# Performance work log

Measured on AMD Instinct MI355X. Metric: run time of the kernel, lower is better.

Reference implementation:

```python
import jax, jax.numpy as jnp
import numpy as np

B, T, C = 4, 2048, 768
H, KVH, D = 6, 6, 128
HALF = D // 2


def setup_inputs() -> dict:
    key = jax.random.key(0)
    ks = jax.random.split(key, 5)
    x = jax.random.normal(ks[0], (B, T, C), dtype=jnp.float32)
    # true rotary frequencies
    inv_freq = 1.0 / (10000.0 ** (jnp.arange(HALF, dtype=jnp.float32) / HALF))
    ang = jnp.arange(T, dtype=jnp.float32)[:, None] * inv_freq[None, :]  # [T, HALF]
    cos, sin = jnp.cos(ang), jnp.sin(ang)
    s = 0.02
    wq = jax.random.normal(ks[1], (H * D, C), dtype=jnp.float32) * s
    wk = jax.random.normal(ks[2], (KVH * D, C), dtype=jnp.float32) * s
    wv = jax.random.normal(ks[3], (KVH * D, C), dtype=jnp.float32) * s
    wproj = jax.random.normal(ks[4], (C, C), dtype=jnp.float32) * s
    return {"x": x, "cos": cos, "sin": sin, "wq": wq, "wk": wk, "wv": wv, "wproj": wproj}


def _norm(t, eps=1e-6):
    # torch: (x - mean) / (std + eps), std unbiased (ddof=1)
    mean = jnp.mean(t, axis=-1, keepdims=True)
    var = jnp.sum((t - mean) ** 2, axis=-1, keepdims=True) / (t.shape[-1] - 1)
    return (t - mean) / (jnp.sqrt(var) + eps)


def _rope(t, cos, sin):
    # t: [B, T, heads, D]; cos/sin: [T, HALF]
    x1, x2 = t[..., :HALF], t[..., HALF:]
    c = cos[None, :, None, :]
    s = sin[None, :, None, :]
    return jnp.concatenate([x1 * c + x2 * s, -x1 * s + x2 * c], axis=-1)


def reference(x, cos, sin, wq, wk, wv, wproj):
    q = jnp.einsum('btc,oc->bto', x, wq).reshape(B, T, H, D)
    k = jnp.einsum('btc,oc->bto', x, wk).reshape(B, T, KVH, D)
    v = jnp.einsum('btc,oc->bto', x, wv).reshape(B, T, KVH, D)
    q = _norm(_rope(q, cos, sin))
    k = _norm(_rope(k, cos, sin))
    # -> [B, heads, T, D]
    q = q.transpose(0, 2, 1, 3)
    k = k.transpose(0, 2, 1, 3)
    v = v.transpose(0, 2, 1, 3)
    # nrep = H // KVH == 1, repeat_kv is a no-op here
    scale = 1.0 / jnp.sqrt(jnp.float32(D))
    scores = jnp.einsum('bhtd,bhsd->bhts', q, k) * scale  # [B,H,T,T]
    causal = jnp.tril(jnp.ones((T, T), dtype=bool))
    scores = jnp.where(causal[None, None], scores, jnp.float32(-1e30))
    attn = jax.nn.softmax(scores, axis=-1)
    y = jnp.einsum('bhts,bhsd->bhtd', attn, v)
    y = y.transpose(0, 2, 1, 3).reshape(B, T, H * D)
    return jnp.einsum('bto,co->btc', y, wproj)
```

## Files before the change

### kernel.cpp

```cpp
#include <hip/hip_runtime.h>

#define BB 4
#define TT 2048
#define CC 768
#define HH 6
#define DD 128
#define BT (BB * TT)
#define HALF 64
#define NBH (BB * HH)
#define QKSCALE 0.12753785627919282f

typedef __bf16 v8bf __attribute__((ext_vector_type(8)));
typedef float f32x4 __attribute__((ext_vector_type(4)));

__device__ __forceinline__ unsigned short f2b(float f) {
  union { float f; unsigned u; } v; v.f = f;
  unsigned r = v.u + 0x7FFFu + ((v.u >> 16) & 1u);
  return (unsigned short)(r >> 16);
}
__device__ __forceinline__ float b2f(unsigned short u) {
  union { unsigned u; float f; } v; v.u = (unsigned)u << 16;
  return v.f;
}
__device__ __forceinline__ unsigned pk2(float f0, float f1) {
  union { float f; unsigned u; } a, b; a.f = f1; b.f = f0;
  return __builtin_amdgcn_perm(a.u, b.u, 0x07060302u);
}
__device__ __forceinline__ float ex2(float x) {
  float r; asm("v_exp_f32 %0, %1" : "=v"(r) : "v"(x)); return r;
}

__device__ __forceinline__ void load_lds16(const void* g, void* l) {
  __builtin_amdgcn_global_load_lds(
      (const __attribute__((address_space(1))) unsigned int*)g,
      (__attribute__((address_space(3))) unsigned int*)(unsigned int)(unsigned long long)(l),
      16, 0, 0);
}

__global__ __launch_bounds__(256) void cvt_all_kernel(const float* __restrict__ x,
                                                      const float* __restrict__ w0,
                                                      const float* __restrict__ w1,
                                                      const float* __restrict__ w2,
                                                      const float* __restrict__ w3,
                                                      unsigned short* __restrict__ xb,
                                                      unsigned short* __restrict__ wb) {
  int bx = blockIdx.x;
  const float* src;
  unsigned short* dst;
  int i;
  if (bx < 6144) {
    src = x; dst = xb; i = bx * 256 + threadIdx.x;
  } else {
    int bsel = (bx - 6144) / 576;
    src = bsel == 0 ? w0 : bsel == 1 ? w1 : bsel == 2 ? w2 : w3;
    dst = wb + bsel * 589824;
    i = ((bx - 6144) % 576) * 256 + threadIdx.x;
  }
  float4 f = ((const float4*)src)[i];
  ushort4 o;
  o.x = f2b(f.x); o.y = f2b(f.y); o.z = f2b(f.z); o.w = f2b(f.w);
  ((ushort4*)dst)[i] = o;
}

__global__ __launch_bounds__(256) void gemm_qkv(const unsigned short* __restrict__ A,
                                                const unsigned short* __restrict__ Wall,
                                                unsigned short* __restrict__ qb,
                                                unsigned short* __restrict__ kb,
                                                unsigned short* __restrict__ vt) {
  __shared__ __align__(16) unsigned short As[2][512 * 8];
  __shared__ __align__(16) unsigned short Bs[2][512 * 8];
  const int m0 = blockIdx.x * 128;
  const int wsel = blockIdx.y / HH, h = blockIdx.y % HH;
  const unsigned short* W = Wall + (size_t)wsel * 589824 + (size_t)h * 128 * CC;
  const int tid = threadIdx.x;
  const int wave = tid >> 6, lane = tid & 63;
  const int fr = lane & 15, quad = lane >> 4;
  const int wm = (wave & 1) * 64, wn = (wave >> 1) * 64;

  f32x4 acc[4][4];
#pragma unroll
  for (int i = 0; i < 4; i++)
#pragma unroll
    for (int j = 0; j < 4; j++) acc[i][j] = (f32x4){0.f, 0.f, 0.f, 0.f};

  auto stage = [&](int kk, int buf) {
#pragma unroll
    for (int it = 0; it < 2; it++) {
      int base_slot = wave * 128 + it * 64;
      int sigma = base_slot + lane;
      int r = sigma >> 2, g = (sigma & 3) ^ ((r >> 1) & 3);
      load_lds16(A + (size_t)(m0 + r) * CC + kk + g * 8, &As[buf][base_slot * 8]);
      load_lds16(W + (size_t)r * CC + kk + g * 8, &Bs[buf][base_slot * 8]);
    }
  };

  stage(0, 0);
  __syncthreads();
  for (int step = 0; step < CC / 32; step++) {
    int buf = step & 1;
    if (step + 1 < CC / 32) stage((step + 1) * 32, buf ^ 1);
    v8bf af[4], bfr[4];
#pragma unroll
    for (int i = 0; i < 4; i++) {
      int ra = wm + i * 16 + fr;
      af[i] = *(const v8bf*)&As[buf][(4 * ra + (quad ^ ((ra >> 1) & 3))) * 8];
      int rb = wn + i * 16 + fr;
      bfr[i] = *(const v8bf*)&Bs[buf][(4 * rb + (quad ^ ((rb >> 1) & 3))) * 8];
    }
#pragma unroll
    for (int i = 0; i < 4; i++)
#pragma unroll
      for (int j = 0; j < 4; j++)
        acc[i][j] = __builtin_amdgcn_mfma_f32_16x16x32_bf16(af[i], bfr[j], acc[i][j], 0, 0, 0);
    __syncthreads();
  }

  if (wsel < 2) {
    unsigned short* dst = wsel ? kb : qb;
#pragma unroll
    for (int i = 0; i < 4; i++) {
      int rr0 = m0 + wm + i * 16 + quad * 4;
      int b = rr0 >> 11, t0 = rr0 & 2047;
      size_t base = ((size_t)(b * HH + h) * TT + t0) * DD;
#pragma unroll
      for (int j = 0; j < 4; j++) {
        int d = wn + j * 16 + fr;
#pragma unroll
        for (int r = 0; r < 4; r++)
          dst[base + (size_t)r * DD + d] = f2b(acc[i][j][r]);
      }
    }
  } else {
#pragma unroll
    for (int i = 0; i < 4; i++) {
      int rr0 = m0 + wm + i * 16 + quad * 4;
      int b = rr0 >> 11, t0_ = rr0 & 2047;
      int bh = b * HH + h;
      int jt = t0_ >> 5;
      int qv = (t0_ >> 3) & 3;
      int jj = t0_ & 7;
#pragma unroll
      for (int j = 0; j < 4; j++) {
        int d = wn + j * 16 + fr;
        int lane_v = qv * 16 + (d & 15);
        size_t off = ((size_t)(bh * 64 + jt) * 8 + (d >> 4)) * 512 + lane_v * 8 + jj;
        ushort4 u = { f2b(acc[i][j][0]), f2b(acc[i][j][1]),
                      f2b(acc[i][j][2]), f2b(acc[i][j][3]) };
        *(ushort4*)&vt[off] = u;
      }
    }
  }
}

__global__ __launch_bounds__(256) void gemm_w64(const unsigned short* __restrict__ A,
                                                const unsigned short* __restrict__ W,
                                                float* __restrict__ C) {
  __shared__ __align__(16) unsigned short As[2][256 * 8];
  __shared__ __align__(16) unsigned short Bs[2][512 * 8];
  const int m0 = blockIdx.x * 64, n0 = blockIdx.y * 128;
  const int tid = threadIdx.x;
  const int wave = tid >> 6, lane = tid & 63;
  const int fr = lane & 15, quad = lane >> 4;
  const int wm = (wave & 1) * 32, wn = (wave >> 1) * 64;

  f32x4 acc[2][4];
#pragma unroll
  for (int i = 0; i < 2; i++)
#pragma unroll
    for (int j = 0; j < 4; j++) acc[i][j] = (f32x4){0.f, 0.f, 0.f, 0.f};

  auto stage = [&](int kk, int buf) {
    {
      int base_slot = wave * 64;
      int sigma = base_slot + lane;
      int r = sigma >> 2, g = (sigma & 3) ^ ((r >> 1) & 3);
      load_lds16(A + (size_t)(m0 + r) * CC + kk + g * 8, &As[buf][base_slot * 8]);
    }
#pragma unroll
    for (int it = 0; it < 2; it++) {
      int base_slot = wave * 128 + it * 64;
      int sigma = base_slot + lane;
      int r = sigma >> 2, g = (sigma & 3) ^ ((r >> 1) & 3);
      load_lds16(W + (size_t)(n0 + r) * CC + kk + g * 8, &Bs[buf][base_slot * 8]);
    }
  };

  stage(0, 0);
  __syncthreads();
  for (int step = 0; step < CC / 32; step++) {
    int buf = step & 1;
    if (step + 1 < CC / 32) stage((step + 1) * 32, buf ^ 1);
    v8bf af[2], bfr[4];
#pragma unroll
    for (int i = 0; i < 2; i++) {
      int ra = wm + i * 16 + fr;
      af[i] = *(const v8bf*)&As[buf][(4 * ra + (quad ^ ((ra >> 1) & 3))) * 8];
    }
#pragma unroll
    for (int j = 0; j < 4; j++) {
      int rb = wn + j * 16 + fr;
      bfr[j] = *(const v8bf*)&Bs[buf][(4 * rb + (quad ^ ((rb >> 1) & 3))) * 8];
    }
#pragma unroll
    for (int i = 0; i < 2; i++)
#pragma unroll
      for (int j = 0; j < 4; j++)
        acc[i][j] = __builtin_amdgcn_mfma_f32_16x16x32_bf16(af[i], bfr[j], acc[i][j], 0, 0, 0);
    __syncthreads();
  }

  const int orow = m0 + wm + quad * 4;
#pragma unroll
  for (int i = 0; i < 2; i++)
#pragma unroll
    for (int j = 0; j < 4; j++) {
      int oc = n0 + wn + j * 16 + fr;
#pragma unroll
      for (int r = 0; r < 4; r++)
        C[(size_t)(orow + i * 16 + r) * CC + oc] = acc[i][j][r];
    }
}

__global__ __launch_bounds__(256) void rope_all_kernel(unsigned short* __restrict__ qb,
                                                       const unsigned short* __restrict__ kb,
                                                       const float* __restrict__ cosb,
                                                       const float* __restrict__ sinb,
                                                       unsigned short* __restrict__ k2) {
  int bx = blockIdx.x;
  bool isq = (bx < 12288);
  const unsigned short* src = isq ? qb : kb;
  float scale = isq ? QKSCALE : 1.0f;
  int idx = (bx % 12288) * 4 + (threadIdx.x >> 6);
  int lane = threadIdx.x & 63;
  int tpos = idx & (TT - 1);
  size_t base = (size_t)idx * DD;

  float x1 = b2f(src[base + lane]);
  float x2 = b2f(src[base + HALF + lane]);
  float c = cosb[tpos * HALF + lane];
  float s = sinb[tpos * HALF + lane];
  float o1 = x1 * c + x2 * s;
  float o2 = x2 * c - x1 * s;

  float sum = o1 + o2;
#pragma unroll
  for (int off = 32; off; off >>= 1) sum += __shfl_xor(sum, off);
  float mean = sum * (1.f / 128.f);
  float d1 = o1 - mean, d2 = o2 - mean;
  float vs = d1 * d1 + d2 * d2;
#pragma unroll
  for (int off = 32; off; off >>= 1) vs += __shfl_xor(vs, off);
  float inv = scale / (sqrtf(vs * (1.f / 127.f)) + 1e-6f);

  if (isq) {
    qb[base + lane] = f2b(d1 * inv);
    qb[base + HALF + lane] = f2b(d2 * inv);
  } else {
    int bh = idx >> 11, t = idx & 2047;
    int jt = t >> 5, rr = t & 31;
    int half = rr >> 4, frv = rr & 15;
    int q5 = (lane >> 3) & 3, j = lane & 7, kb1 = lane >> 5;
    size_t b2 = (size_t)bh * 262144 + (size_t)jt * 4096 + half * 512 + q5 * 128 + frv * 8 + j;
    k2[b2 + (size_t)kb1 * 1024] = f2b(d1 * inv);
    k2[b2 + (size_t)(kb1 + 2) * 1024] = f2b(d2 * inv);
  }
}

__global__ __launch_bounds__(256) void attn_mfma(const unsigned short* __restrict__ qtb,
                                                 const unsigned short* __restrict__ k2b,
                                                 const unsigned short* __restrict__ v2b,
                                                 unsigned short* __restrict__ Opart,
                                                 float* __restrict__ lpart) {
  const int u = blockIdx.x;
  const int bh = u % NBH;
  const int uu = u / NBH;
  int qt, c;
  if (uu < 16)      { qt = 15 - (uu >> 2); c = uu & 3; }
  else if (uu < 28) { int k = uu - 16; int q3 = k / 3; qt = 11 - q3; c = k - q3 * 3; }
  else if (uu < 36) { int k = uu - 28; qt = 7 - (k >> 1); c = k & 1; }
  else              { qt = 3 - (uu - 36); c = 0; }
  const int t0 = c * 16;
  const int t1 = min(t0 + 16, 4 * qt + 4);
  const int niter = t1 - t0;

  const int tid = threadIdx.x;
  const int wave = tid >> 6, lane = tid & 63;
  const int fr = lane & 15, quad = lane >> 4;
  const int idxf = 4 * ((quad & 1) * 32 + fr);
  const int idxs = idxf + 64;
  const size_t head_base = (size_t)bh * TT * DD;
  const int m0 = qt * 128 + wave * 32;

  const unsigned short* k2h = k2b + (size_t)bh * 262144;
  const unsigned short* v2h = v2b + (size_t)bh * 262144;

  v8bf qf[2][4];
#pragma unroll
  for (int qs = 0; qs < 2; qs++)
#pragma unroll
    for (int kbk = 0; kbk < 4; kbk++)
      qf[qs][kbk] = *(const v8bf*)(qtb + head_base +
                                   (size_t)(m0 + qs * 16 + fr) * DD + kbk * 32 + quad * 8);

  const __bf16 one_bf = (__bf16)1.0f;
  v8bf ones = {one_bf, one_bf, one_bf, one_bf, one_bf, one_bf, one_bf, one_bf};

  f32x4 oacc[2][8];
#pragma unroll
  for (int qs = 0; qs < 2; qs++)
#pragma unroll
    for (int i = 0; i < 8; i++) oacc[qs][i] = (f32x4){0.f, 0.f, 0.f, 0.f};
  f32x4 lacc[2] = {(f32x4){0.f, 0.f, 0.f, 0.f}, (f32x4){0.f, 0.f, 0.f, 0.f}};

  for (int it = 0; it < niter; it++) {
    const int jt = t0 + it;
    const int j0 = jt * 32;
    if (j0 > m0 + 31) continue;

    const unsigned short* kp = k2h + (size_t)jt * 4096 + lane * 8;
    v8bf kf[8];
#pragma unroll
    for (int i = 0; i < 8; i++) kf[i] = *(const v8bf*)&kp[i * 512];
    const unsigned short* vp = v2h + (size_t)jt * 4096 + lane * 8;
    v8bf vf[8];
#pragma unroll
    for (int i = 0; i < 8; i++) vf[i] = *(const v8bf*)&vp[i * 512];

    f32x4 st[2][2];
#pragma unroll
    for (int qs = 0; qs < 2; qs++) { st[qs][0] = (f32x4){0,0,0,0}; st[qs][1] = (f32x4){0,0,0,0}; }
    __builtin_amdgcn_s_setprio(1);
#pragma unroll
    for (int kbk = 0; kbk < 4; kbk++) {
      st[0][0] = __builtin_amdgcn_mfma_f32_16x16x32_bf16(kf[kbk * 2],     qf[0][kbk], st[0][0], 0, 0, 0);
      st[0][1] = __builtin_amdgcn_mfma_f32_16x16x32_bf16(kf[kbk * 2 + 1], qf[0][kbk], st[0][1], 0, 0, 0);
      st[1][0] = __builtin_amdgcn_mfma_f32_16x16x32_bf16(kf[kbk * 2],     qf[1][kbk], st[1][0], 0, 0, 0);
      st[1][1] = __builtin_amdgcn_mfma_f32_16x16x32_bf16(kf[kbk * 2 + 1], qf[1][kbk], st[1][1], 0, 0, 0);
    }
    __builtin_amdgcn_s_setprio(0);

    const bool diag = (j0 + 31 > m0);
    v8bf pa0, pa1;
#pragma unroll
    for (int qs = 0; qs < 2; qs++) {
      float p[8];
      if (diag) {
        const int qrow = m0 + qs * 16 + fr;
#pragma unroll
        for (int r = 0; r < 4; r++) {
          int c0 = j0 + quad * 4 + r;
          p[r]     = (c0      <= qrow) ? ex2(st[qs][0][r]) : 0.f;
          p[4 + r] = (c0 + 16 <= qrow) ? ex2(st[qs][1][r]) : 0.f;
        }
      } else {
#pragma unroll
        for (int r = 0; r < 4; r++) { p[r] = ex2(st[qs][0][r]); p[4 + r] = ex2(st[qs][1][r]); }
      }
      unsigned A0 = pk2(p[0], p[1]), A1 = pk2(p[2], p[3]);
      unsigned B0 = pk2(p[4], p[5]), B1 = pk2(p[6], p[7]);
      unsigned alo0 = (unsigned)__builtin_amdgcn_ds_bpermute(idxf, (int)A0);
      unsigned alo1 = (unsigned)__builtin_amdgcn_ds_bpermute(idxf, (int)A1);
      unsigned ahi0 = (unsigned)__builtin_amdgcn_ds_bpermute(idxs, (int)A0);
      unsigned ahi1 = (unsigned)__builtin_amdgcn_ds_bpermute(idxs, (int)A1);
      unsigned blo0 = (unsigned)__builtin_amdgcn_ds_bpermute(idxf, (int)B0);
      unsigned blo1 = (unsigned)__builtin_amdgcn_ds_bpermute(idxf, (int)B1);
      unsigned bhi0 = (unsigned)__builtin_amdgcn_ds_bpermute(idxs, (int)B0);
      unsigned bhi1 = (unsigned)__builtin_amdgcn_ds_bpermute(idxs, (int)B1);
      const bool ql = (quad < 2);
      union { unsigned w[4]; v8bf v; } pw;
      pw.w[0] = ql ? alo0 : blo0;
      pw.w[1] = ql ? alo1 : blo1;
      pw.w[2] = ql ? ahi0 : bhi0;
      pw.w[3] = ql ? ahi1 : bhi1;
      if (qs == 0) pa0 = pw.v; else pa1 = pw.v;
    }

    __builtin_amdgcn_s_setprio(1);
#pragma unroll
    for (int nt2 = 0; nt2 < 8; nt2++) {
      oacc[0][nt2] = __builtin_amdgcn_mfma_f32_16x16x32_bf16(pa0, vf[nt2], oacc[0][nt2], 0, 0, 0);
      oacc[1][nt2] = __builtin_amdgcn_mfma_f32_16x16x32_bf16(pa1, vf[nt2], oacc[1][nt2], 0, 0, 0);
    }
    lacc[0] = __builtin_amdgcn_mfma_f32_16x16x32_bf16(pa0, ones, lacc[0], 0, 0, 0);
    lacc[1] = __builtin_amdgcn_mfma_f32_16x16x32_bf16(pa1, ones, lacc[1], 0, 0, 0);
    __builtin_amdgcn_s_setprio(0);
  }

  unsigned short* Oc = Opart + (size_t)c * (NBH * TT * DD) + head_base;
#pragma unroll
  for (int qs = 0; qs < 2; qs++) {
#pragma unroll
    for (int nt2 = 0; nt2 < 8; nt2++)
#pragma unroll
      for (int r = 0; r < 4; r++)
        Oc[(size_t)(m0 + qs * 16 + quad * 4 + r) * DD + nt2 * 16 + fr] = f2b(oacc[qs][nt2][r]);
    if (fr == 0) {
#pragma unroll
      for (int r = 0; r < 4; r++)
        lpart[c * (NBH * TT) + bh * TT + m0 + qs * 16 + quad * 4 + r] = lacc[qs][r];
    }
  }
}

__global__ __launch_bounds__(256) void combine_kernel(const unsigned short* __restrict__ Opart,
                                                      const float* __restrict__ lpart,
                                                      unsigned short* __restrict__ yb) {
  int idx = blockIdx.x * 256 + threadIdx.x;
  int row = idx >> 5;
  int dg = (idx & 31) * 4;
  int t = row & 2047;
  int qt = t >> 7;
  int nc = (4 * qt + 4 + 15) >> 4;

  float a0 = 0.f, a1 = 0.f, a2 = 0.f, a3 = 0.f, l = 0.f;
  for (int cchunk = 0; cchunk < nc; cchunk++) {
    ushort4 o = *(const ushort4*)&Opart[(size_t)cchunk * (NBH * TT * DD) + (size_t)row * DD + dg];
    a0 += b2f(o.x); a1 += b2f(o.y); a2 += b2f(o.z); a3 += b2f(o.w);
    l += lpart[cchunk * (NBH * TT) + row];
  }
  float linv = 1.f / l;
  int bh = row >> 11;
  int b = bh / HH, h = bh % HH;
  ushort4 uo = { f2b(a0 * linv), f2b(a1 * linv), f2b(a2 * linv), f2b(a3 * linv) };
  *(ushort4*)&yb[((size_t)(b * TT + t)) * CC + h * DD + dg] = uo;
}

extern "C" void kernel_launch(void* const* d_in, const int* in_sizes, int n_in,
                              void* d_out, int out_size, void* d_ws, size_t ws_size,
                              hipStream_t stream) {
  const float* x     = (const float*)d_in[0];
  const float* cosb  = (const float*)d_in[1];
  const float* sinb  = (const float*)d_in[2];
  const float* wq    = (const float*)d_in[3];
  const float* wk    = (const float*)d_in[4];
  const float* wv    = (const float*)d_in[5];
  const float* wproj = (const float*)d_in[6];
  float* out = (float*)d_out;

  char* w = (char*)d_ws;
  unsigned short* q_t   = (unsigned short*)(w);
  unsigned short* k_t   = (unsigned short*)(w + 12582912);
  float*          lpart = (float*)(w + 12582912);
  unsigned short* v_t   = (unsigned short*)(w + 25165824);
  unsigned short* yb    = (unsigned short*)(w + 37748736);
  unsigned short* xb    = (unsigned short*)(w + 50331648);
  unsigned short* K2    = (unsigned short*)(w + 50331648);
  unsigned short* wb    = (unsigned short*)(w + 62914560);
  unsigned short* Opart = (unsigned short*)(w + 67633152);

  cvt_all_kernel<<<8448, 256, 0, stream>>>(x, wq, wk, wv, wproj, xb, wb);

  gemm_qkv<<<dim3(BT / 128, 3 * HH), 256, 0, stream>>>(xb, wb, q_t, k_t, v_t);

  rope_all_kernel<<<24576, 256, 0, stream>>>(q_t, k_t, cosb, sinb, K2);

  attn_mfma<<<960, 256, 0, stream>>>(q_t, K2, v_t, Opart, lpart);
  combine_kernel<<<6144, 256, 0, stream>>>(Opart, lpart, yb);

  gemm_w64<<<dim3(BT / 64, CC / 128), 256, 0, stream>>>(yb, wb + 3 * 589824, out);
}
```

Measured before the change: 232.4 us.

## Halve attention query tile to 64 rows and reorder causal chunk schedule

Each attention block now handles 64 query rows (16 per wave, one MFMA row subtile) instead of 128. The grid grows from 960 to 1920 blocks, with a new block-to-(query block, key chunk) mapping that issues the longest work first. The aim is finer causal granularity and better load balance across CUs. In exchange, each K/V fragment loaded from global memory now serves half as many query rows, so K/V traffic roughly doubles and there is less MFMA work per load.

```diff
diff --git a/kernel.cpp b/kernel.cpp
--- a/kernel.cpp
+++ b/kernel.cpp
@@ -274,13 +274,14 @@
   const int u = blockIdx.x;
   const int bh = u % NBH;
   const int uu = u / NBH;
-  int qt, c;
-  if (uu < 16)      { qt = 15 - (uu >> 2); c = uu & 3; }
-  else if (uu < 28) { int k = uu - 16; int q3 = k / 3; qt = 11 - q3; c = k - q3 * 3; }
-  else if (uu < 36) { int k = uu - 28; qt = 7 - (k >> 1); c = k & 1; }
-  else              { qt = 3 - (uu - 36); c = 0; }
+  int qb, c;
+  if (uu < 25)       { c = 0; qb = 31 - uu; }
+  else if (uu < 42)  { c = 1; qb = 31 - (uu - 25); }
+  else if (uu < 51)  { c = 2; qb = 31 - (uu - 42); }
+  else if (uu == 51) { c = 3; qb = 31; }
+  else { int uu2 = uu - 52; int sidx = uu2 >> 2; c = uu2 & 3; qb = 8 * c + 6 - sidx; }
   const int t0 = c * 16;
-  const int t1 = min(t0 + 16, 4 * qt + 4);
+  const int t1 = min(t0 + 16, 2 * qb + 2);
   const int niter = t1 - t0;
 
   const int tid = threadIdx.x;
@@ -289,33 +290,29 @@
   const int idxf = 4 * ((quad & 1) * 32 + fr);
   const int idxs = idxf + 64;
   const size_t head_base = (size_t)bh * TT * DD;
-  const int m0 = qt * 128 + wave * 32;
+  const int m0 = qb * 64 + wave * 16;
 
   const unsigned short* k2h = k2b + (size_t)bh * 262144;
   const unsigned short* v2h = v2b + (size_t)bh * 262144;
 
-  v8bf qf[2][4];
-#pragma unroll
-  for (int qs = 0; qs < 2; qs++)
-#pragma unroll
-    for (int kbk = 0; kbk < 4; kbk++)
-      qf[qs][kbk] = *(const v8bf*)(qtb + head_base +
-                                   (size_t)(m0 + qs * 16 + fr) * DD + kbk * 32 + quad * 8);
+  v8bf qf[4];
+#pragma unroll
+  for (int kbk = 0; kbk < 4; kbk++)
+    qf[kbk] = *(const v8bf*)(qtb + head_base +
+                             (size_t)(m0 + fr) * DD + kbk * 32 + quad * 8);
 
   const __bf16 one_bf = (__bf16)1.0f;
   v8bf ones = {one_bf, one_bf, one_bf, one_bf, one_bf, one_bf, one_bf, one_bf};
 
-  f32x4 oacc[2][8];
-#pragma unroll
-  for (int qs = 0; qs < 2; qs++)
-#pragma unroll
-    for (int i = 0; i < 8; i++) oacc[qs][i] = (f32x4){0.f, 0.f, 0.f, 0.f};
-  f32x4 lacc[2] = {(f32x4){0.f, 0.f, 0.f, 0.f}, (f32x4){0.f, 0.f, 0.f, 0.f}};
+  f32x4 oacc[8];
+#pragma unroll
+  for (int i = 0; i < 8; i++) oacc[i] = (f32x4){0.f, 0.f, 0.f, 0.f};
+  f32x4 lacc = (f32x4){0.f, 0.f, 0.f, 0.f};
 
   for (int it = 0; it < niter; it++) {
     const int jt = t0 + it;
     const int j0 = jt * 32;
-    if (j0 > m0 + 31) continue;
+    if (j0 > m0 + 15) continue;
 
     const unsigned short* kp = k2h + (size_t)jt * 4096 + lane * 8;
     v8bf kf[8];
@@ -326,79 +323,66 @@
 #pragma unroll
     for (int i = 0; i < 8; i++) vf[i] = *(const v8bf*)&vp[i * 512];
 
-    f32x4 st[2][2];
-#pragma unroll
-    for (int qs = 0; qs < 2; qs++) { st[qs][0] = (f32x4){0,0,0,0}; st[qs][1] = (f32x4){0,0,0,0}; }
+    f32x4 st0 = (f32x4){0.f, 0.f, 0.f, 0.f};
+    f32x4 st1 = (f32x4){0.f, 0.f, 0.f, 0.f};
     __builtin_amdgcn_s_setprio(1);
 #pragma unroll
     for (int kbk = 0; kbk < 4; kbk++) {
-      st[0][0] = __builtin_amdgcn_mfma_f32_16x16x32_bf16(kf[kbk * 2],     qf[0][kbk], st[0][0], 0, 0, 0);
-      st[0][1] = __builtin_amdgcn_mfma_f32_16x16x32_bf16(kf[kbk * 2 + 1], qf[0][kbk], st[0][1], 0, 0, 0);
-      st[1][0] = __builtin_amdgcn_mfma_f32_16x16x32_bf16(kf[kbk * 2],     qf[1][kbk], st[1][0], 0, 0, 0);
-      st[1][1] = __builtin_amdgcn_mfma_f32_16x16x32_bf16(kf[kbk * 2 + 1], qf[1][kbk], st[1][1], 0, 0, 0);
+      st0 = __builtin_amdgcn_mfma_f32_16x16x32_bf16(kf[kbk * 2],     qf[kbk], st0, 0, 0, 0);
+      st1 = __builtin_amdgcn_mfma_f32_16x16x32_bf16(kf[kbk * 2 + 1], qf[kbk], st1, 0, 0, 0);
     }
     __builtin_amdgcn_s_setprio(0);
 
     const bool diag = (j0 + 31 > m0);
-    v8bf pa0, pa1;
-#pragma unroll
-    for (int qs = 0; qs < 2; qs++) {
-      float p[8];
-      if (diag) {
-        const int qrow = m0 + qs * 16 + fr;
-#pragma unroll
-        for (int r = 0; r < 4; r++) {
-          int c0 = j0 + quad * 4 + r;
-          p[r]     = (c0      <= qrow) ? ex2(st[qs][0][r]) : 0.f;
-          p[4 + r] = (c0 + 16 <= qrow) ? ex2(st[qs][1][r]) : 0.f;
-        }
-      } else {
-#pragma unroll
-        for (int r = 0; r < 4; r++) { p[r] = ex2(st[qs][0][r]); p[4 + r] = ex2(st[qs][1][r]); }
+    float p[8];
+    if (diag) {
+      const int qrow = m0 + fr;
+#pragma unroll
+      for (int r = 0; r < 4; r++) {
+        int c0 = j0 + quad * 4 + r;
+        p[r]     = (c0      <= qrow) ? ex2(st0[r]) : 0.f;
+        p[4 + r] = (c0 + 16 <= qrow) ? ex2(st1[r]) : 0.f;
       }
-      unsigned A0 = pk2(p[0], p[1]), A1 = pk2(p[2], p[3]);
-      unsigned B0 = pk2(p[4], p[5]), B1 = pk2(p[6], p[7]);
-      unsigned alo0 = (unsigned)__builtin_amdgcn_ds_bpermute(idxf, (int)A0);
-      unsigned alo1 = (unsigned)__builtin_amdgcn_ds_bpermute(idxf, (int)A1);
-      unsigned ahi0 = (unsigned)__builtin_amdgcn_ds_bpermute(idxs, (int)A0);
-      unsigned ahi1 = (unsigned)__builtin_amdgcn_ds_bpermute(idxs, (int)A1);
-      unsigned blo0 = (unsigned)__builtin_amdgcn_ds_bpermute(idxf, (int)B0);
-      unsigned blo1 = (unsigned)__builtin_amdgcn_ds_bpermute(idxf, (int)B1);
-      unsigned bhi0 = (unsigned)__builtin_amdgcn_ds_bpermute(idxs, (int)B0);
-      unsigned bhi1 = (unsigned)__builtin_amdgcn_ds_bpermute(idxs, (int)B1);
-      const bool ql = (quad < 2);
-      union { unsigned w[4]; v8bf v; } pw;
-      pw.w[0] = ql ? alo0 : blo0;
-      pw.w[1] = ql ? alo1 : blo1;
-      pw.w[2] = ql ? ahi0 : bhi0;
-      pw.w[3] = ql ? ahi1 : bhi1;
-      if (qs == 0) pa0 = pw.v; else pa1 = pw.v;
-    }
+    } else {
+#pragma unroll
+      for (int r = 0; r < 4; r++) { p[r] = ex2(st0[r]); p[4 + r] = ex2(st1[r]); }
+    }
+    unsigned A0 = pk2(p[0], p[1]), A1 = pk2(p[2], p[3]);
+    unsigned B0 = pk2(p[4], p[5]), B1 = pk2(p[6], p[7]);
+    unsigned alo0 = (unsigned)__builtin_amdgcn_ds_bpermute(idxf, (int)A0);
+    unsigned alo1 = (unsigned)__builtin_amdgcn_ds_bpermute(idxf, (int)A1);
+    unsigned ahi0 = (unsigned)__builtin_amdgcn_ds_bpermute(idxs, (int)A0);
+    unsigned ahi1 = (unsigned)__builtin_amdgcn_ds_bpermute(idxs, (int)A1);
+    unsigned blo0 = (unsigned)__builtin_amdgcn_ds_bpermute(idxf, (int)B0);
+    unsigned blo1 = (unsigned)__builtin_amdgcn_ds_bpermute(idxf, (int)B1);
+    unsigned bhi0 = (unsigned)__builtin_amdgcn_ds_bpermute(idxs, (int)B0);
+    unsigned bhi1 = (unsigned)__builtin_amdgcn_ds_bpermute(idxs, (int)B1);
+    const bool ql = (quad < 2);
+    union { unsigned w[4]; v8bf v; } pw;
+    pw.w[0] = ql ? alo0 : blo0;
+    pw.w[1] = ql ? alo1 : blo1;
+    pw.w[2] = ql ? ahi0 : bhi0;
+    pw.w[3] = ql ? ahi1 : bhi1;
+    v8bf pa = pw.v;
 
     __builtin_amdgcn_s_setprio(1);
 #pragma unroll
-    for (int nt2 = 0; nt2 < 8; nt2++) {
-      oacc[0][nt2] = __builtin_amdgcn_mfma_f32_16x16x32_bf16(pa0, vf[nt2], oacc[0][nt2], 0, 0, 0);
-      oacc[1][nt2] = __builtin_amdgcn_mfma_f32_16x16x32_bf16(pa1, vf[nt2], oacc[1][nt2], 0, 0, 0);
-    }
-    lacc[0] = __builtin_amdgcn_mfma_f32_16x16x32_bf16(pa0, ones, lacc[0], 0, 0, 0);
-    lacc[1] = __builtin_amdgcn_mfma_f32_16x16x32_bf16(pa1, ones, lacc[1], 0, 0, 0);
+    for (int nt2 = 0; nt2 < 8; nt2++)
+      oacc[nt2] = __builtin_amdgcn_mfma_f32_16x16x32_bf16(pa, vf[nt2], oacc[nt2], 0, 0, 0);
+    lacc = __builtin_amdgcn_mfma_f32_16x16x32_bf16(pa, ones, lacc, 0, 0, 0);
     __builtin_amdgcn_s_setprio(0);
   }
 
   unsigned short* Oc = Opart + (size_t)c * (NBH * TT * DD) + head_base;
 #pragma unroll
-  for (int qs = 0; qs < 2; qs++) {
-#pragma unroll
-    for (int nt2 = 0; nt2 < 8; nt2++)
-#pragma unroll
-      for (int r = 0; r < 4; r++)
-        Oc[(size_t)(m0 + qs * 16 + quad * 4 + r) * DD + nt2 * 16 + fr] = f2b(oacc[qs][nt2][r]);
-    if (fr == 0) {
-#pragma unroll
-      for (int r = 0; r < 4; r++)
-        lpart[c * (NBH * TT) + bh * TT + m0 + qs * 16 + quad * 4 + r] = lacc[qs][r];
-    }
+  for (int nt2 = 0; nt2 < 8; nt2++)
+#pragma unroll
+    for (int r = 0; r < 4; r++)
+      Oc[(size_t)(m0 + quad * 4 + r) * DD + nt2 * 16 + fr] = f2b(oacc[nt2][r]);
+  if (fr == 0) {
+#pragma unroll
+    for (int r = 0; r < 4; r++)
+      lpart[c * (NBH * TT) + bh * TT + m0 + quad * 4 + r] = lacc[r];
   }
 }
 
@@ -454,7 +438,7 @@
 
   rope_all_kernel<<<24576, 256, 0, stream>>>(q_t, k_t, cosb, sinb, K2);
 
-  attn_mfma<<<960, 256, 0, stream>>>(q_t, K2, v_t, Opart, lpart);
+  attn_mfma<<<1920, 256, 0, stream>>>(q_t, K2, v_t, Opart, lpart);
   combine_kernel<<<6144, 256, 0, stream>>>(Opart, lpart, yb);
 
   gemm_w64<<<dim3(BT / 64, CC / 128), 256, 0, stream>>>(yb, wb + 3 * 589824, out);
```

New measurement: 241.7 us. 4.0% more time.

## Double query rows per attention wave and rebalance the split-K work table

Applied to the files above, without the earlier changes.

Each wave now handles 64 query rows instead of 32, so every K/V tile loaded from memory feeds twice as many MFMAs. Block count is halved and the causal split-K schedule becomes a constant lookup table keyed to 256-row query blocks, with the combine kernel's chunk count updated to match. Partial-output stores become nontemporal. Register pressure roughly doubles for the accumulators and the launch bound is set to one block, which may lower occupancy and latency hiding. Fewer blocks may also leave compute units idle.

```diff
diff --git a/kernel.cpp b/kernel.cpp
--- a/kernel.cpp
+++ b/kernel.cpp
@@ -266,21 +266,20 @@
   }
 }
 
-__global__ __launch_bounds__(256) void attn_mfma(const unsigned short* __restrict__ qtb,
-                                                 const unsigned short* __restrict__ k2b,
-                                                 const unsigned short* __restrict__ v2b,
-                                                 unsigned short* __restrict__ Opart,
-                                                 float* __restrict__ lpart) {
+__constant__ unsigned char qb_tab[20] = {1,2,3,4,5,6,7, 3,4,5,6,7, 5,6,7, 7, 0,2,4,6};
+__constant__ unsigned char c_tab[20]  = {0,0,0,0,0,0,0, 1,1,1,1,1, 2,2,2, 3, 0,1,2,3};
+
+__global__ __launch_bounds__(256, 1) void attn_mfma(const unsigned short* __restrict__ qtb,
+                                                    const unsigned short* __restrict__ k2b,
+                                                    const unsigned short* __restrict__ v2b,
+                                                    unsigned short* __restrict__ Opart,
+                                                    float* __restrict__ lpart) {
   const int u = blockIdx.x;
   const int bh = u % NBH;
   const int uu = u / NBH;
-  int qt, c;
-  if (uu < 16)      { qt = 15 - (uu >> 2); c = uu & 3; }
-  else if (uu < 28) { int k = uu - 16; int q3 = k / 3; qt = 11 - q3; c = k - q3 * 3; }
-  else if (uu < 36) { int k = uu - 28; qt = 7 - (k >> 1); c = k & 1; }
-  else              { qt = 3 - (uu - 36); c = 0; }
+  const int qb = (int)qb_tab[uu], c = (int)c_tab[uu];
   const int t0 = c * 16;
-  const int t1 = min(t0 + 16, 4 * qt + 4);
+  const int t1 = min(t0 + 16, 8 * qb + 8);
   const int niter = t1 - t0;
 
   const int tid = threadIdx.x;
@@ -289,14 +288,14 @@
   const int idxf = 4 * ((quad & 1) * 32 + fr);
   const int idxs = idxf + 64;
   const size_t head_base = (size_t)bh * TT * DD;
-  const int m0 = qt * 128 + wave * 32;
+  const int m0 = qb * 256 + wave * 64;
 
   const unsigned short* k2h = k2b + (size_t)bh * 262144;
   const unsigned short* v2h = v2b + (size_t)bh * 262144;
 
-  v8bf qf[2][4];
-#pragma unroll
-  for (int qs = 0; qs < 2; qs++)
+  v8bf qf[4][4];
+#pragma unroll
+  for (int qs = 0; qs < 4; qs++)
 #pragma unroll
     for (int kbk = 0; kbk < 4; kbk++)
       qf[qs][kbk] = *(const v8bf*)(qtb + head_base +
@@ -305,17 +304,19 @@
   const __bf16 one_bf = (__bf16)1.0f;
   v8bf ones = {one_bf, one_bf, one_bf, one_bf, one_bf, one_bf, one_bf, one_bf};
 
-  f32x4 oacc[2][8];
-#pragma unroll
-  for (int qs = 0; qs < 2; qs++)
+  f32x4 oacc[4][8];
+#pragma unroll
+  for (int qs = 0; qs < 4; qs++)
 #pragma unroll
     for (int i = 0; i < 8; i++) oacc[qs][i] = (f32x4){0.f, 0.f, 0.f, 0.f};
-  f32x4 lacc[2] = {(f32x4){0.f, 0.f, 0.f, 0.f}, (f32x4){0.f, 0.f, 0.f, 0.f}};
+  f32x4 lacc[4];
+#pragma unroll
+  for (int qs = 0; qs < 4; qs++) lacc[qs] = (f32x4){0.f, 0.f, 0.f, 0.f};
 
   for (int it = 0; it < niter; it++) {
     const int jt = t0 + it;
     const int j0 = jt * 32;
-    if (j0 > m0 + 31) continue;
+    if (j0 > m0 + 63) continue;
 
     const unsigned short* kp = k2h + (size_t)jt * 4096 + lane * 8;
     v8bf kf[8];
@@ -326,23 +327,24 @@
 #pragma unroll
     for (int i = 0; i < 8; i++) vf[i] = *(const v8bf*)&vp[i * 512];
 
-    f32x4 st[2][2];
-#pragma unroll
-    for (int qs = 0; qs < 2; qs++) { st[qs][0] = (f32x4){0,0,0,0}; st[qs][1] = (f32x4){0,0,0,0}; }
+    f32x4 st[4][2];
+#pragma unroll
+    for (int qs = 0; qs < 4; qs++) { st[qs][0] = (f32x4){0,0,0,0}; st[qs][1] = (f32x4){0,0,0,0}; }
     __builtin_amdgcn_s_setprio(1);
 #pragma unroll
     for (int kbk = 0; kbk < 4; kbk++) {
-      st[0][0] = __builtin_amdgcn_mfma_f32_16x16x32_bf16(kf[kbk * 2],     qf[0][kbk], st[0][0], 0, 0, 0);
-      st[0][1] = __builtin_amdgcn_mfma_f32_16x16x32_bf16(kf[kbk * 2 + 1], qf[0][kbk], st[0][1], 0, 0, 0);
-      st[1][0] = __builtin_amdgcn_mfma_f32_16x16x32_bf16(kf[kbk * 2],     qf[1][kbk], st[1][0], 0, 0, 0);
-      st[1][1] = __builtin_amdgcn_mfma_f32_16x16x32_bf16(kf[kbk * 2 + 1], qf[1][kbk], st[1][1], 0, 0, 0);
+#pragma unroll
+      for (int qs = 0; qs < 4; qs++) {
+        st[qs][0] = __builtin_amdgcn_mfma_f32_16x16x32_bf16(kf[kbk * 2],     qf[qs][kbk], st[qs][0], 0, 0, 0);
+        st[qs][1] = __builtin_amdgcn_mfma_f32_16x16x32_bf16(kf[kbk * 2 + 1], qf[qs][kbk], st[qs][1], 0, 0, 0);
+      }
     }
     __builtin_amdgcn_s_setprio(0);
 
     const bool diag = (j0 + 31 > m0);
-    v8bf pa0, pa1;
-#pragma unroll
-    for (int qs = 0; qs < 2; qs++) {
+    v8bf pa[4];
+#pragma unroll
+    for (int qs = 0; qs < 4; qs++) {
       float p[8];
       if (diag) {
         const int qrow = m0 + qs * 16 + fr;
@@ -372,28 +374,31 @@
       pw.w[1] = ql ? alo1 : blo1;
       pw.w[2] = ql ? ahi0 : bhi0;
       pw.w[3] = ql ? ahi1 : bhi1;
-      if (qs == 0) pa0 = pw.v; else pa1 = pw.v;
+      pa[qs] = pw.v;
     }
 
     __builtin_amdgcn_s_setprio(1);
 #pragma unroll
     for (int nt2 = 0; nt2 < 8; nt2++) {
-      oacc[0][nt2] = __builtin_amdgcn_mfma_f32_16x16x32_bf16(pa0, vf[nt2], oacc[0][nt2], 0, 0, 0);
-      oacc[1][nt2] = __builtin_amdgcn_mfma_f32_16x16x32_bf16(pa1, vf[nt2], oacc[1][nt2], 0, 0, 0);
-    }
-    lacc[0] = __builtin_amdgcn_mfma_f32_16x16x32_bf16(pa0, ones, lacc[0], 0, 0, 0);
-    lacc[1] = __builtin_amdgcn_mfma_f32_16x16x32_bf16(pa1, ones, lacc[1], 0, 0, 0);
+#pragma unroll
+      for (int qs = 0; qs < 4; qs++)
+        oacc[qs][nt2] = __builtin_amdgcn_mfma_f32_16x16x32_bf16(pa[qs], vf[nt2], oacc[qs][nt2], 0, 0, 0);
+    }
+#pragma unroll
+    for (int qs = 0; qs < 4; qs++)
+      lacc[qs] = __builtin_amdgcn_mfma_f32_16x16x32_bf16(pa[qs], ones, lacc[qs], 0, 0, 0);
     __builtin_amdgcn_s_setprio(0);
   }
 
   unsigned short* Oc = Opart + (size_t)c * (NBH * TT * DD) + head_base;
 #pragma unroll
-  for (int qs = 0; qs < 2; qs++) {
+  for (int qs = 0; qs < 4; qs++) {
 #pragma unroll
     for (int nt2 = 0; nt2 < 8; nt2++)
 #pragma unroll
       for (int r = 0; r < 4; r++)
-        Oc[(size_t)(m0 + qs * 16 + quad * 4 + r) * DD + nt2 * 16 + fr] = f2b(oacc[qs][nt2][r]);
+        __builtin_nontemporal_store(f2b(oacc[qs][nt2][r]),
+            &Oc[(size_t)(m0 + qs * 16 + quad * 4 + r) * DD + nt2 * 16 + fr]);
     if (fr == 0) {
 #pragma unroll
       for (int r = 0; r < 4; r++)
@@ -409,8 +414,8 @@
   int row = idx >> 5;
   int dg = (idx & 31) * 4;
   int t = row & 2047;
-  int qt = t >> 7;
-  int nc = (4 * qt + 4 + 15) >> 4;
+  int qb = t >> 8;
+  int nc = (8 * qb + 23) >> 4;
 
   float a0 = 0.f, a1 = 0.f, a2 = 0.f, a3 = 0.f, l = 0.f;
   for (int cchunk = 0; cchunk < nc; cchunk++) {
@@ -454,7 +459,7 @@
 
   rope_all_kernel<<<24576, 256, 0, stream>>>(q_t, k_t, cosb, sinb, K2);
 
-  attn_mfma<<<960, 256, 0, stream>>>(q_t, K2, v_t, Opart, lpart);
+  attn_mfma<<<480, 256, 0, stream>>>(q_t, K2, v_t, Opart, lpart);
   combine_kernel<<<6144, 256, 0, stream>>>(Opart, lpart, yb);
 
   gemm_w64<<<dim3(BT / 64, CC / 128), 256, 0, stream>>>(yb, wb + 3 * 589824, out);
```

After: 258.6 us. 11.3% more time.
